# Kernel tuning notes

Hardware: AMD Instinct MI355X
Metric: run time of the kernel (lower is better)

## Reference

```python
import jax, jax.numpy as jnp
import numpy as np

NEG_SLOPE = 0.2
BN_EPS = 1e-5


def _gatv2(x, Wl, Wr, att, b, src, dst, N):
    # PyG GATv2Conv, concat=False: lin_l on source, lin_r on target,
    # e = a^T LeakyReLU(x_l[j] + x_r[i]); softmax over incoming edges of i;
    # out = mean_h( sum_j alpha_ij * x_l[j] ) + bias
    H, C = att.shape
    xl = (x @ Wl).reshape(N, H, C)
    xr = (x @ Wr).reshape(N, H, C)
    e = jax.nn.leaky_relu(xl[src] + xr[dst], NEG_SLOPE)          # [E,H,C]
    score = jnp.einsum('ehc,hc->eh', e, att)                     # [E,H]
    m = jax.ops.segment_max(score, dst, num_segments=N)          # [N,H]
    a = jnp.exp(score - m[dst])
    denom = jax.ops.segment_sum(a, dst, num_segments=N)
    alpha = a / denom[dst]                                       # [E,H]
    out = jax.ops.segment_sum(alpha[..., None] * xl[src], dst, num_segments=N)  # [N,H,C]
    return out.mean(axis=1) + b


def _bn(h, g, be):
    # BatchNorm1d, training-mode statistics (biased variance)
    mu = h.mean(axis=0)
    var = h.var(axis=0)
    return g * (h - mu) * jax.lax.rsqrt(var + BN_EPS) + be


def _gelu(x):
    return jax.nn.gelu(x, approximate=False)


def setup_inputs() -> dict:
    key = jax.random.key(0)
    N, F, HID, LAT, H, E, G = 50000, 64, 64, 64, 4, 800000, 256
    ks = jax.random.split(key, 32)
    d = {}
    d['x'] = jax.random.normal(ks[0], (N, F), dtype=jnp.float32)
    d['edge_src'] = jax.random.randint(ks[1], (E,), 0, N, dtype=jnp.int32)
    d['edge_dst'] = jax.random.randint(ks[2], (E,), 0, N, dtype=jnp.int32)
    d['batch'] = jnp.sort(jax.random.randint(ks[3], (N,), 0, G, dtype=jnp.int32))
    d['num_graphs'] = G
    def lin(k, fi, fo):
        return jax.random.normal(k, (fi, fo), dtype=jnp.float32) / np.sqrt(fi)
    i = 4
    for L, fin in zip((1, 2, 3), (F, HID, HID)):
        d[f'Wl{L}'] = lin(ks[i], fin, H * HID); i += 1
        d[f'Wr{L}'] = lin(ks[i], fin, H * HID); i += 1
        d[f'att{L}'] = jax.random.normal(ks[i], (H, HID), dtype=jnp.float32) / np.sqrt(HID); i += 1
        d[f'b{L}'] = jnp.zeros((HID,), dtype=jnp.float32)
        d[f'g{L}'] = jax.random.uniform(ks[i], (HID,), dtype=jnp.float32, minval=0.5, maxval=1.5); i += 1
        d[f'be{L}'] = 0.1 * jax.random.normal(ks[i], (HID,), dtype=jnp.float32); i += 1
    d['Wmu'] = lin(ks[i], HID, LAT); i += 1
    d['bmu'] = jnp.zeros((LAT,), dtype=jnp.float32)
    d['Wlv'] = lin(ks[i], HID, LAT); i += 1
    d['blv'] = jnp.zeros((LAT,), dtype=jnp.float32)
    return d


def reference(x, edge_src, edge_dst, batch, num_graphs,
              Wl1, Wr1, att1, b1, g1, be1,
              Wl2, Wr2, att2, b2, g2, be2,
              Wl3, Wr3, att3, b3, g3, be3,
              Wmu, bmu, Wlv, blv):
    N = x.shape[0]
    loops = jnp.arange(N, dtype=edge_src.dtype)
    src = jnp.concatenate([edge_src, loops])  # add_self_loops=True (PyG default)
    dst = jnp.concatenate([edge_dst, loops])

    h = _gelu(_bn(_gatv2(x, Wl1, Wr1, att1, b1, src, dst, N), g1, be1))
    h_in = h
    h = _gelu(_bn(_gatv2(h, Wl2, Wr2, att2, b2, src, dst, N), g2, be2)) + h_in
    h_in = h
    h = _gelu(_bn(_gatv2(h, Wl3, Wr3, att3, b3, src, dst, N), g3, be3)) + h_in

    h_pool = jax.ops.segment_sum(h, batch, num_segments=num_graphs)  # global_add_pool
    return (h_pool @ Wmu + bmu, h_pool @ Wlv + blv)
```

## Files before the change

### kernel.cpp

```cpp
#include <hip/hip_runtime.h>
#include <math.h>

typedef __attribute__((ext_vector_type(8))) short bf16x8;
typedef __attribute__((ext_vector_type(4))) float f32x4;
typedef __attribute__((ext_vector_type(2))) float f32x2;

static __device__ __forceinline__ unsigned short f2bf(float f) {
  unsigned u = __float_as_uint(f);
  unsigned r = (u + 0x7FFF + ((u >> 16) & 1)) >> 16;
  return (unsigned short)r;
}

#define DPP_ADD(x, ctrl) \
  ((x) + __int_as_float(__builtin_amdgcn_update_dpp(0, __float_as_int(x), (ctrl), 0xf, 0xf, true)))

#define NSHARD 64
#define NEB 256
#define ECAP 6144


__global__ __launch_bounds__(256) void k_prep(const float* __restrict__ W0, const float* __restrict__ W1,
                                              const float* __restrict__ W2, const float* __restrict__ W3,
                                              const float* __restrict__ W4, const float* __restrict__ W5,
                                              unsigned short* __restrict__ wt,
                                              const int* __restrict__ esrc,
                                              const int* __restrict__ edst,
                                              int* __restrict__ bktcnt,
                                              int2* __restrict__ ebuf, int E, int N) {
  if (blockIdx.x < 384) {
    int gid = blockIdx.x * 256 + threadIdx.x;
    int m = gid >> 14;
    int r = gid & 16383;
    int k = r >> 8;
    int n = r & 255;
    const float* W = (m == 0) ? W0 : (m == 1) ? W1 : (m == 2) ? W2
                   : (m == 3) ? W3 : (m == 4) ? W4 : W5;
    wt[(size_t)m * 16384 + n * 64 + k] = f2bf(W[k * 256 + n]);
    return;
  }
  const int b = blockIdx.x - 384;
  const int nbk = (N + 255) >> 8;
  __shared__ int cnt[256], base[256];
  cnt[threadIdx.x] = 0;
  __syncthreads();
  const int chunk = (E + NEB - 1) / NEB;
  const int e0 = b * chunk, e1 = min(e0 + chunk, E);
  for (int e = e0 + threadIdx.x; e < e1; e += 256) atomicAdd(&cnt[edst[e] >> 8], 1);
  __syncthreads();
  if (threadIdx.x < nbk && cnt[threadIdx.x])
    base[threadIdx.x] = atomicAdd(&bktcnt[threadIdx.x], cnt[threadIdx.x]);
  cnt[threadIdx.x] = 0;
  __syncthreads();
  for (int e = e0 + threadIdx.x; e < e1; e += 256) {
    int d = edst[e];
    int bk = d >> 8;
    int p = base[bk] + atomicAdd(&cnt[bk], 1);
    ebuf[(size_t)bk * ECAP + p] = make_int2(d, esrc[e]);
  }
}


static __device__ __forceinline__ void csr_pass2(const int2* __restrict__ ebuf,
                                                 const int* __restrict__ bktcnt,
                                                 int* __restrict__ rowptr,
                                                 int* __restrict__ colb,
                                                 int* __restrict__ ccur,
                                                 int N, char* smem) {
  const int b = blockIdx.x;
  const int nbk = (N + 255) >> 8;
  if (b >= nbk) return;
  int* hist = (int*)smem;
  int* s = (int*)smem + 256;
  int* sb = (int*)smem + 512;
  const int tid = threadIdx.x;
  const int lo = b * ECAP;
  const int hi = lo + bktcnt[b];
  hist[tid] = 0;
  __syncthreads();
  for (int i = lo + tid; i < hi; i += 256) atomicAdd(&hist[ebuf[i].x & 255], 1);
  __syncthreads();
  int deg = hist[tid];
  int pd = (deg + 3) & ~3;
  s[tid] = pd;
  __syncthreads();
  for (int off = 1; off < 256; off <<= 1) {
    int t = (tid >= off) ? s[tid - off] : 0;
    __syncthreads();
    s[tid] += t;
    __syncthreads();
  }
  if (tid == 255) sb[0] = atomicAdd(ccur, s[255]);
  __syncthreads();
  int pos = sb[0] + s[tid] - pd;
  int node = (b << 8) + tid;
  if (node < N) rowptr[node] = (int)((unsigned)pos | ((unsigned)deg << 22));
  hist[tid] = pos;
  __syncthreads();
  for (int i = lo + tid; i < hi; i += 256) {
    int2 e = ebuf[i];
    int p = atomicAdd(&hist[e.x & 255], 1);
    colb[p] = e.y << 8;
  }
}


static __device__ __forceinline__ void mm_gemm(const float* __restrict__ src,
                                               const float* __restrict__ bnsums,
                                               const float* __restrict__ g,
                                               const float* __restrict__ be,
                                               const float* __restrict__ resid,
                                               float* __restrict__ hout,
                                               const unsigned short* __restrict__ wt,
                                               unsigned char* __restrict__ xlb,
                                               unsigned char* __restrict__ xrb,
                                               int N, int ntiles, float inv_n,
                                               char* smem) {
  unsigned short* Bs = (unsigned short*)smem;
  unsigned short* Ah = (unsigned short*)(smem + 32768);
  const int t = threadIdx.x;
  const unsigned short* wb = wt + (blockIdx.y ? 16384 : 0);
  unsigned char* dst = blockIdx.y ? xrb : xlb;

  const int wave = t >> 6, lane = t & 63;
  const int rw = (wave & 1) * 16, cw = (wave >> 1) * 128;
  const int m15 = lane & 15, quad = lane >> 4;
  const int arow = t >> 3, ac0 = (t & 7) * 8;
  const int aoff = arow * 64 + (((t & 7) ^ (arow & 7)) << 3);

  float scale[8], shift[8];
  if (bnsums) {
    float* stat = (float*)smem;
    if (t < 128) {
      float a = 0.f;
#pragma unroll
      for (int sd = 0; sd < NSHARD; ++sd) a += bnsums[sd * 128 + t];
      stat[t] = a;
    }
    __syncthreads();
#pragma unroll
    for (int i = 0; i < 8; ++i) {
      int c = ac0 + i;
      float mu = stat[c] * inv_n;
      float var = stat[64 + c] * inv_n - mu * mu;
      float rs = rsqrtf(var + 1e-5f) * g[c];
      scale[i] = rs;
      shift[i] = be[c] - mu * rs;
    }
    __syncthreads();
  }

#pragma unroll
  for (int j = 0; j < 8; ++j) {
    int cidx = t + 256 * j;
    int n = cidx >> 3, gg = cidx & 7;
    *(bf16x8*)&Bs[n * 64 + (((gg ^ ((n >> 3) & 7))) << 3)] =
        *(const bf16x8*)(wb + (size_t)n * 64 + gg * 8);
  }

  const bool wr_h = (hout != nullptr) && (blockIdx.y == 0);
  const int gstride = gridDim.x;

  float4 a0, a1, rv0, rv1;
  auto loadA = [&](int tl, float4& x0, float4& x1, float4& r0v, float4& r1v) {
    x0 = make_float4(0.f, 0.f, 0.f, 0.f);
    x1 = make_float4(0.f, 0.f, 0.f, 0.f);
    r0v = make_float4(0.f, 0.f, 0.f, 0.f);
    r1v = make_float4(0.f, 0.f, 0.f, 0.f);
    int gr = tl * 32 + arow;
    if (tl < ntiles && gr < N) {
      x0 = *(const float4*)(src + (size_t)gr * 64 + ac0);
      x1 = *(const float4*)(src + (size_t)gr * 64 + ac0 + 4);
      if (resid) {
        r0v = *(const float4*)(resid + (size_t)gr * 64 + ac0);
        r1v = *(const float4*)(resid + (size_t)gr * 64 + ac0 + 4);
      }
    }
  };
  loadA(blockIdx.x, a0, a1, rv0, rv1);

  for (int tile = blockIdx.x; tile < ntiles; tile += gstride) {
    int r0 = tile * 32;
    int gr = r0 + arow;
    {
      float vs[8] = {a0.x, a0.y, a0.z, a0.w, a1.x, a1.y, a1.z, a1.w};
      if (bnsums) {
        float rv[8] = {rv0.x, rv0.y, rv0.z, rv0.w, rv1.x, rv1.y, rv1.z, rv1.w};
#pragma unroll
        for (int i = 0; i < 8; ++i) {
          float v = fmaf(vs[i], scale[i], shift[i]);
          float ge = 0.5f * v * (1.f + erff(v * 0.70710678118654752f));
          vs[i] = ge + rv[i];
        }
        if (wr_h && gr < N) {
          float4 o0 = {vs[0], vs[1], vs[2], vs[3]};
          float4 o1 = {vs[4], vs[5], vs[6], vs[7]};
          *(float4*)(hout + (size_t)gr * 64 + ac0) = o0;
          *(float4*)(hout + (size_t)gr * 64 + ac0 + 4) = o1;
        }
      }
      bf16x8 hi8;
#pragma unroll
      for (int i = 0; i < 8; ++i) hi8[i] = (short)f2bf(vs[i]);
      *(bf16x8*)&Ah[aoff] = hi8;
    }
    __syncthreads();

    loadA(tile + gstride, a0, a1, rv0, rv1);

    f32x4 acc[8];
#pragma unroll
    for (int s = 0; s < 8; ++s) acc[s] = (f32x4){0.f, 0.f, 0.f, 0.f};
    const int xq = m15 & 7;
#pragma unroll
    for (int kk = 0; kk < 64; kk += 32) {
      const int ga = (((kk >> 3) + quad) ^ xq) << 3;
      bf16x8 ah = *(const bf16x8*)&Ah[(rw + m15) * 64 + ga];
#pragma unroll
      for (int s = 0; s < 8; ++s) {
        bf16x8 b = *(const bf16x8*)&Bs[(cw + m15 * 8 + s) * 64 + ga];
        acc[s] = __builtin_amdgcn_mfma_f32_16x16x32_bf16(ah, b, acc[s], 0, 0, 0);
      }
    }
#pragma unroll
    for (int r = 0; r < 4; ++r) {
      int row_g = r0 + rw + quad * 4 + r;
      if (row_g < N) {
        int w0 = __builtin_amdgcn_cvt_pk_fp8_f32(acc[0][r], acc[1][r], 0, false);
        w0 = __builtin_amdgcn_cvt_pk_fp8_f32(acc[2][r], acc[3][r], w0, true);
        int w1 = __builtin_amdgcn_cvt_pk_fp8_f32(acc[4][r], acc[5][r], 0, false);
        w1 = __builtin_amdgcn_cvt_pk_fp8_f32(acc[6][r], acc[7][r], w1, true);
        uint2 o = {(unsigned)w0, (unsigned)w1};
        *(uint2*)(dst + (size_t)row_g * 256 + cw + m15 * 8) = o;
      }
    }
    __syncthreads();
  }
}

__global__ __launch_bounds__(256, 4) void k_mm0(const float* __restrict__ src,
                                                const unsigned short* __restrict__ wt,
                                                unsigned char* __restrict__ xlb,
                                                unsigned char* __restrict__ xrb,
                                                const int2* __restrict__ ebuf,
                                                const int* __restrict__ bktcnt,
                                                int* __restrict__ rowptr,
                                                int* __restrict__ colb,
                                                int* __restrict__ ccur,
                                                int N, int ntiles) {
  __shared__ __align__(16) char smem[36864];
  if (blockIdx.y == 2) {
    csr_pass2(ebuf, bktcnt, rowptr, colb, ccur, N, smem);
    return;
  }
  mm_gemm(src, nullptr, nullptr, nullptr, nullptr, nullptr, wt, xlb, xrb, N, ntiles, 0.f, smem);
}

__global__ __launch_bounds__(256, 4) void k_mm1(const float* __restrict__ src,
                                                const float* __restrict__ bnsums,
                                                const float* __restrict__ g,
                                                const float* __restrict__ be,
                                                float* __restrict__ hout,
                                                const unsigned short* __restrict__ wt,
                                                unsigned char* __restrict__ xlb,
                                                unsigned char* __restrict__ xrb,
                                                int N, int ntiles, float inv_n) {
  __shared__ __align__(16) char smem[36864];
  mm_gemm(src, bnsums, g, be, nullptr, hout, wt, xlb, xrb, N, ntiles, inv_n, smem);
}

__global__ __launch_bounds__(256, 4) void k_mm2(const float* __restrict__ src,
                                                const float* __restrict__ bnsums,
                                                const float* __restrict__ g,
                                                const float* __restrict__ be,
                                                const float* __restrict__ resid,
                                                float* __restrict__ hout,
                                                const unsigned short* __restrict__ wt,
                                                unsigned char* __restrict__ xlb,
                                                unsigned char* __restrict__ xrb,
                                                int N, int ntiles, float inv_n) {
  __shared__ __align__(16) char smem[36864];
  mm_gemm(src, bnsums, g, be, resid, hout, wt, xlb, xrb, N, ntiles, inv_n, smem);
}


static __device__ __forceinline__ void gat_body(const unsigned char* __restrict__ xlb,
                                                const unsigned char* __restrict__ xrb,
                                                const float* __restrict__ att,
                                                const float* __restrict__ bias,
                                                const int* __restrict__ rowptr,
                                                const int* __restrict__ colb,
                                                float* __restrict__ out,
                                                float* __restrict__ bnsums, int N) {
  __shared__ float sres[4][64];
  const int lane = threadIdx.x & 63;
  const int wv = threadIdx.x >> 6;
  const int half = lane >> 5;
  const int l5 = lane & 31;
  const int node0 = blockIdx.x * 4 + wv;
  const bool valid = node0 < N;
  const int node = __builtin_amdgcn_readfirstlane(valid ? node0 : 0);
  const int rp = rowptr[node];
  const int beg = rp & 0x3FFFFF;
  const int deg = (int)(((unsigned)rp) >> 22);
  const int end = valid ? beg + deg : beg;

  const unsigned char* xl = xlb;
  const unsigned lb = (unsigned)l5 * 8u;

  auto sel = [&](int a, int b) { return (unsigned)(half ? b : a); };

  int4 c0 = *(const int4*)(colb + beg);
  int4 c1 = *(const int4*)(colb + beg + 4);
  const unsigned self_off = (unsigned)(node << 8);
  uint2 vbs = *(const uint2*)(xl + self_off + lb);
  uint2 pd0 = *(const uint2*)(xl + (sel(c0.x, c0.y) + lb));
  uint2 pd1 = *(const uint2*)(xl + (sel(c0.z, c0.w) + lb));
  uint2 pt0 = *(const uint2*)(xl + (sel(c1.x, c1.y) + lb));
  uint2 pt1 = *(const uint2*)(xl + (sel(c1.z, c1.w) + lb));
  int4 cn = *(const int4*)(colb + beg + 8);

  float4 aa = *(const float4*)(att + l5 * 8);
  float4 ab = *(const float4*)(att + l5 * 8 + 4);
  const float LOG2E = 1.4426950408889634f;
  const f32x2 a01 = {aa.x * LOG2E, aa.y * LOG2E};
  const f32x2 a23 = {aa.z * LOG2E, aa.w * LOG2E};
  const f32x2 a45 = {ab.x * LOG2E, ab.y * LOG2E};
  const f32x2 a67 = {ab.z * LOG2E, ab.w * LOG2E};
  const f32x2 c02 = {0.2f, 0.2f};
  uint2 xru = *(const uint2*)(xrb + self_off + lb);
  const f32x2 xr01 = __builtin_amdgcn_cvt_pk_f32_fp8((int)xru.x, false);
  const f32x2 xr23 = __builtin_amdgcn_cvt_pk_f32_fp8((int)xru.x, true);
  const f32x2 xr45 = __builtin_amdgcn_cvt_pk_f32_fp8((int)xru.y, false);
  const f32x2 xr67 = __builtin_amdgcn_cvt_pk_f32_fp8((int)xru.y, true);

  auto score = [&](uint2 vb, f32x2& v01, f32x2& v23, f32x2& v45, f32x2& v67) -> float {
    v01 = __builtin_amdgcn_cvt_pk_f32_fp8((int)vb.x, false);
    v23 = __builtin_amdgcn_cvt_pk_f32_fp8((int)vb.x, true);
    v45 = __builtin_amdgcn_cvt_pk_f32_fp8((int)vb.y, false);
    v67 = __builtin_amdgcn_cvt_pk_f32_fp8((int)vb.y, true);
    f32x2 s01 = v01 + xr01;
    f32x2 s23 = v23 + xr23;
    f32x2 s45 = v45 + xr45;
    f32x2 s67 = v67 + xr67;
    s01 = __builtin_elementwise_max(s01, s01 * c02);
    s23 = __builtin_elementwise_max(s23, s23 * c02);
    s45 = __builtin_elementwise_max(s45, s45 * c02);
    s67 = __builtin_elementwise_max(s67, s67 * c02);
    f32x2 q = s01 * a01;
    q = __builtin_elementwise_fma(s23, a23, q);
    q = __builtin_elementwise_fma(s45, a45, q);
    q = __builtin_elementwise_fma(s67, a67, q);
    float p = q.x + q.y;
    p = DPP_ADD(p, 0xB1);
    p = DPP_ADD(p, 0x4E);
    p = DPP_ADD(p, 0x141);
    return p;
  };

  f32x2 sv01, sv23, sv45, sv67;
  const float m = score(vbs, sv01, sv23, sv45, sv67);

  const float hsel = half ? 0.f : 1.f;
  float lsum = hsel;
  const f32x2 hs2 = {hsel, hsel};
  f32x2 o01 = sv01 * hs2, o23 = sv23 * hs2, o45 = sv45 * hs2, o67 = sv67 * hs2;

  auto proc = [&](uint2 vb, int ebase) {
    f32x2 v01, v23, v45, v67;
    float p = score(vb, v01, v23, v45, v67);
    float w = __builtin_amdgcn_exp2f(fminf(p - m, 126.f));
    w = (ebase + half < end) ? w : 0.f;
    lsum += w;
    f32x2 w2 = {w, w};
    o01 = __builtin_elementwise_fma(w2, v01, o01);
    o23 = __builtin_elementwise_fma(w2, v23, o23);
    o45 = __builtin_elementwise_fma(w2, v45, o45);
    o67 = __builtin_elementwise_fma(w2, v67, o67);
  };

  for (int e = beg; e < end; e += 4) {
    uint2 pu0 = *(const uint2*)(xl + (sel(cn.x, cn.y) + lb));
    uint2 pu1 = *(const uint2*)(xl + (sel(cn.z, cn.w) + lb));
    cn = *(const int4*)(colb + e + 12);
    proc(pd0, e);
    proc(pd1, e + 2);
    pd0 = pt0; pd1 = pt1;
    pt0 = pu0; pt1 = pu1;
  }

  lsum += __shfl_xor(lsum, 32, 64);
  float inv = __builtin_amdgcn_rcpf(lsum);
  float r[8] = {o01.x * inv, o01.y * inv, o23.x * inv, o23.y * inv,
                o45.x * inv, o45.y * inv, o67.x * inv, o67.y * inv};
#pragma unroll
  for (int j = 0; j < 8; ++j) {
    r[j] += __shfl_xor(r[j], 8, 64);
    r[j] += __shfl_xor(r[j], 16, 64);
    r[j] += __shfl_xor(r[j], 32, 64);
  }
  if (lane < 8) {
    float4 res0 = {0.f, 0.f, 0.f, 0.f}, res1 = {0.f, 0.f, 0.f, 0.f};
    if (valid) {
      float4 b0 = *(const float4*)(bias + lane * 8);
      float4 b1 = *(const float4*)(bias + lane * 8 + 4);
      res0.x = 0.25f * r[0] + b0.x;
      res0.y = 0.25f * r[1] + b0.y;
      res0.z = 0.25f * r[2] + b0.z;
      res0.w = 0.25f * r[3] + b0.w;
      res1.x = 0.25f * r[4] + b1.x;
      res1.y = 0.25f * r[5] + b1.y;
      res1.z = 0.25f * r[6] + b1.z;
      res1.w = 0.25f * r[7] + b1.w;
      *(float4*)(out + (size_t)node * 64 + lane * 8) = res0;
      *(float4*)(out + (size_t)node * 64 + lane * 8 + 4) = res1;
    }
    *(float4*)&sres[wv][lane * 8] = res0;
    *(float4*)&sres[wv][lane * 8 + 4] = res1;
  }
  __syncthreads();
  if (threadIdx.x < 64) {
    int c = threadIdx.x;
    float s0 = sres[0][c], s1 = sres[1][c], s2 = sres[2][c], s3 = sres[3][c];
    float* bs = bnsums + (size_t)(blockIdx.x & (NSHARD - 1)) * 128;
    atomicAdd(&bs[c], s0 + s1 + s2 + s3);
    atomicAdd(&bs[64 + c], s0 * s0 + s1 * s1 + s2 * s2 + s3 * s3);
  }
}

__global__ __launch_bounds__(256) void k_gat0(const unsigned char* __restrict__ xlb,
                                              const unsigned char* __restrict__ xrb,
                                              const float* __restrict__ att,
                                              const float* __restrict__ bias,
                                              const int* __restrict__ rowptr,
                                              const int* __restrict__ colb,
                                              float* __restrict__ out,
                                              float* __restrict__ bnsums, int N) {
  gat_body(xlb, xrb, att, bias, rowptr, colb, out, bnsums, N);
}
__global__ __launch_bounds__(256) void k_gat1(const unsigned char* __restrict__ xlb,
                                              const unsigned char* __restrict__ xrb,
                                              const float* __restrict__ att,
                                              const float* __restrict__ bias,
                                              const int* __restrict__ rowptr,
                                              const int* __restrict__ colb,
                                              float* __restrict__ out,
                                              float* __restrict__ bnsums, int N) {
  gat_body(xlb, xrb, att, bias, rowptr, colb, out, bnsums, N);
}
__global__ __launch_bounds__(256) void k_gat2(const unsigned char* __restrict__ xlb,
                                              const unsigned char* __restrict__ xrb,
                                              const float* __restrict__ att,
                                              const float* __restrict__ bias,
                                              const int* __restrict__ rowptr,
                                              const int* __restrict__ colb,
                                              float* __restrict__ out,
                                              float* __restrict__ bnsums, int N) {
  gat_body(xlb, xrb, att, bias, rowptr, colb, out, bnsums, N);
}


__global__ __launch_bounds__(256) void k_bn_pool(const float* __restrict__ gat,
                                                 const float* __restrict__ bnsums,
                                                 const float* __restrict__ g,
                                                 const float* __restrict__ be,
                                                 const float* __restrict__ resid,
                                                 const int* __restrict__ batch,
                                                 float* __restrict__ pool,
                                                 int N, float inv_n) {
  __shared__ float sc[64], sh[64];
  if (threadIdx.x < 64) {
    int c = threadIdx.x;
    float s = 0.f, q = 0.f;
    for (int sd = 0; sd < NSHARD; ++sd) {
      s += bnsums[sd * 128 + c];
      q += bnsums[sd * 128 + 64 + c];
    }
    float mu = s * inv_n;
    float var = q * inv_n - mu * mu;
    float rs = rsqrtf(var + 1e-5f) * g[c];
    sc[c] = rs;
    sh[c] = be[c] - mu * rs;
  }
  __syncthreads();
  const int c = threadIdx.x & 63;
  const int wv = threadIdx.x >> 6;
  int n0 = (blockIdx.x * 4 + wv) * 32;
  if (n0 >= N) return;
  int n1 = min(n0 + 32, N);
  int curg = batch[n0];
  float acc = 0.f;
  for (int n = n0; n < n1; ++n) {
    int b = batch[n];
    if (b != curg) {
      atomicAdd(&pool[(size_t)curg * 64 + c], acc);
      acc = 0.f;
      curg = b;
    }
    float v = fmaf(gat[(size_t)n * 64 + c], sc[c], sh[c]);
    float ge = 0.5f * v * (1.f + erff(v * 0.70710678118654752f));
    acc += ge + resid[(size_t)n * 64 + c];
  }
  atomicAdd(&pool[(size_t)curg * 64 + c], acc);
}


__global__ void k_head(const float* __restrict__ pool, const float* __restrict__ Wmu,
                       const float* __restrict__ bmu, const float* __restrict__ Wlv,
                       const float* __restrict__ blv, float* __restrict__ out, int G) {
  int g = blockIdx.x;
  int c = threadIdx.x;
  __shared__ float row[64];
  row[c] = pool[(size_t)g * 64 + c];
  __syncthreads();
  float am = 0.f, al = 0.f;
  for (int k = 0; k < 64; ++k) {
    float r = row[k];
    am = fmaf(r, Wmu[k * 64 + c], am);
    al = fmaf(r, Wlv[k * 64 + c], al);
  }
  out[(size_t)g * 64 + c] = am + bmu[c];
  out[(size_t)G * 64 + (size_t)g * 64 + c] = al + blv[c];
}


extern "C" void kernel_launch(void* const* d_in, const int* in_sizes, int n_in,
                              void* d_out, int out_size, void* d_ws, size_t ws_size,
                              hipStream_t stream) {
  const float* x    = (const float*)d_in[0];
  const int* esrc   = (const int*)d_in[1];
  const int* edst   = (const int*)d_in[2];
  const int* batch  = (const int*)d_in[3];
  const float* Wl[3]  = {(const float*)d_in[5],  (const float*)d_in[11], (const float*)d_in[17]};
  const float* Wr[3]  = {(const float*)d_in[6],  (const float*)d_in[12], (const float*)d_in[18]};
  const float* att[3] = {(const float*)d_in[7],  (const float*)d_in[13], (const float*)d_in[19]};
  const float* bia[3] = {(const float*)d_in[8],  (const float*)d_in[14], (const float*)d_in[20]};
  const float* gam[3] = {(const float*)d_in[9],  (const float*)d_in[15], (const float*)d_in[21]};
  const float* bet[3] = {(const float*)d_in[10], (const float*)d_in[16], (const float*)d_in[22]};
  const float* Wmu = (const float*)d_in[23];
  const float* bmu = (const float*)d_in[24];
  const float* Wlv = (const float*)d_in[25];
  const float* blv = (const float*)d_in[26];
  float* out = (float*)d_out;

  const int N = in_sizes[0] / 64;
  const int E = in_sizes[1];
  const int G = out_size / 128;
  const int nbk = (N + 255) / 256;

  char* p = (char*)d_ws;
  auto alloc = [&](size_t bytes) -> void* {
    void* r = (void*)p;
    p += (bytes + 255) & ~(size_t)255;
    return r;
  };
  int*   bktcnt  = (int*)alloc(256 * 4);
  float* bnsums  = (float*)alloc(3 * NSHARD * 128 * 4);
  float* pool    = (float*)alloc((size_t)G * 64 * 4);
  int*   ccur    = (int*)alloc(256);
  int*   colb    = (int*)alloc(((size_t)E + 3 * (size_t)N + 64) * 4);
  char*  zend    = p;
  unsigned char* xlb = (unsigned char*)alloc((size_t)N * 256);
  unsigned char* xrb = (unsigned char*)alloc((size_t)N * 256);
  float* hA     = (float*)alloc((size_t)N * 64 * 4);
  float* hB     = (float*)alloc((size_t)N * 64 * 4);
  float* gat    = (float*)alloc((size_t)N * 64 * 4);
  int*   rowptr = (int*)alloc((size_t)(N + 1) * 4);
  int2*  ebuf   = (int2*)alloc((size_t)nbk * ECAP * 8);
  unsigned short* wt = (unsigned short*)alloc(6 * 16384 * 2);

  const int nbGat = (N + 3) / 4;
  const int ntiles = (N + 31) / 32;
  const float inv_n = 1.f / (float)N;

  hipMemsetAsync(bktcnt, 0, (size_t)(zend - (char*)bktcnt), stream);

  k_prep<<<384 + NEB, 256, 0, stream>>>(Wl[0], Wr[0], Wl[1], Wr[1], Wl[2], Wr[2], wt,
                                        esrc, edst, bktcnt, ebuf, E, N);

  float* bns0 = bnsums;
  float* bns1 = bnsums + NSHARD * 128;
  float* bns2 = bnsums + 2 * NSHARD * 128;

  k_mm0<<<dim3(512, 3), 256, 0, stream>>>(x, wt, xlb, xrb, ebuf, bktcnt, rowptr, colb,
                                          ccur, N, ntiles);
  k_gat0<<<nbGat, 256, 0, stream>>>(xlb, xrb, att[0], bia[0], rowptr, colb, gat, bns0, N);
  k_mm1<<<dim3(512, 2), 256, 0, stream>>>(gat, bns0, gam[0], bet[0], hA,
                                          wt + 2 * 16384, xlb, xrb, N, ntiles, inv_n);
  k_gat1<<<nbGat, 256, 0, stream>>>(xlb, xrb, att[1], bia[1], rowptr, colb, gat, bns1, N);
  k_mm2<<<dim3(512, 2), 256, 0, stream>>>(gat, bns1, gam[1], bet[1], hA, hB,
                                          wt + 4 * 16384, xlb, xrb, N, ntiles, inv_n);
  k_gat2<<<nbGat, 256, 0, stream>>>(xlb, xrb, att[2], bia[2], rowptr, colb, gat, bns2, N);
  k_bn_pool<<<(N + 127) / 128, 256, 0, stream>>>(gat, bns2, gam[2], bet[2], hB, batch, pool,
                                                 N, inv_n);
  k_head<<<G, 64, 0, stream>>>(pool, Wmu, bmu, Wlv, blv, out, G);
}
```

Before: 358.1 us.

## Fuse left and right projection GEMMs into one block pass

Each GEMM block now loads both the Wl and Wr weight tiles into shared memory and computes xl and xr together from a single staged A tile. Previously the two projections ran as separate grid-y slices, and each slice re-read the input and redid the BN/GELU/residual preprocessing. This halves the A-side loads and the normalization work. In exchange, shared memory per block doubles to about 68KB, launch bounds drop to 2 blocks per CU, and the accumulator register count doubles.

```diff
diff --git a/kernel.cpp b/kernel.cpp
--- a/kernel.cpp
+++ b/kernel.cpp
@@ -116,10 +116,8 @@
                                                int N, int ntiles, float inv_n,
                                                char* smem) {
   unsigned short* Bs = (unsigned short*)smem;
-  unsigned short* Ah = (unsigned short*)(smem + 32768);
+  unsigned short* Ah = (unsigned short*)(smem + 65536);
   const int t = threadIdx.x;
-  const unsigned short* wb = wt + (blockIdx.y ? 16384 : 0);
-  unsigned char* dst = blockIdx.y ? xrb : xlb;
 
   const int wave = t >> 6, lane = t & 63;
   const int rw = (wave & 1) * 16, cw = (wave >> 1) * 128;
@@ -150,14 +148,14 @@
   }
 
 #pragma unroll
-  for (int j = 0; j < 8; ++j) {
+  for (int j = 0; j < 16; ++j) {
     int cidx = t + 256 * j;
     int n = cidx >> 3, gg = cidx & 7;
     *(bf16x8*)&Bs[n * 64 + (((gg ^ ((n >> 3) & 7))) << 3)] =
-        *(const bf16x8*)(wb + (size_t)n * 64 + gg * 8);
-  }
-
-  const bool wr_h = (hout != nullptr) && (blockIdx.y == 0);
+        *(const bf16x8*)(wt + (size_t)n * 64 + gg * 8);
+  }
+
+  const bool wr_h = (hout != nullptr);
   const int gstride = gridDim.x;
 
   float4 a0, a1, rv0, rv1;
@@ -207,9 +205,12 @@
 
     loadA(tile + gstride, a0, a1, rv0, rv1);
 
-    f32x4 acc[8];
-#pragma unroll
-    for (int s = 0; s < 8; ++s) acc[s] = (f32x4){0.f, 0.f, 0.f, 0.f};
+    f32x4 accL[8], accR[8];
+#pragma unroll
+    for (int s = 0; s < 8; ++s) {
+      accL[s] = (f32x4){0.f, 0.f, 0.f, 0.f};
+      accR[s] = (f32x4){0.f, 0.f, 0.f, 0.f};
+    }
     const int xq = m15 & 7;
 #pragma unroll
     for (int kk = 0; kk < 64; kk += 32) {
@@ -217,27 +218,35 @@
       bf16x8 ah = *(const bf16x8*)&Ah[(rw + m15) * 64 + ga];
 #pragma unroll
       for (int s = 0; s < 8; ++s) {
-        bf16x8 b = *(const bf16x8*)&Bs[(cw + m15 * 8 + s) * 64 + ga];
-        acc[s] = __builtin_amdgcn_mfma_f32_16x16x32_bf16(ah, b, acc[s], 0, 0, 0);
+        bf16x8 bl = *(const bf16x8*)&Bs[(cw + m15 * 8 + s) * 64 + ga];
+        accL[s] = __builtin_amdgcn_mfma_f32_16x16x32_bf16(ah, bl, accL[s], 0, 0, 0);
+        bf16x8 br = *(const bf16x8*)&Bs[(256 + cw + m15 * 8 + s) * 64 + ga];
+        accR[s] = __builtin_amdgcn_mfma_f32_16x16x32_bf16(ah, br, accR[s], 0, 0, 0);
       }
     }
 #pragma unroll
     for (int r = 0; r < 4; ++r) {
       int row_g = r0 + rw + quad * 4 + r;
       if (row_g < N) {
-        int w0 = __builtin_amdgcn_cvt_pk_fp8_f32(acc[0][r], acc[1][r], 0, false);
-        w0 = __builtin_amdgcn_cvt_pk_fp8_f32(acc[2][r], acc[3][r], w0, true);
-        int w1 = __builtin_amdgcn_cvt_pk_fp8_f32(acc[4][r], acc[5][r], 0, false);
-        w1 = __builtin_amdgcn_cvt_pk_fp8_f32(acc[6][r], acc[7][r], w1, true);
-        uint2 o = {(unsigned)w0, (unsigned)w1};
-        *(uint2*)(dst + (size_t)row_g * 256 + cw + m15 * 8) = o;
+        int w0 = __builtin_amdgcn_cvt_pk_fp8_f32(accL[0][r], accL[1][r], 0, false);
+        w0 = __builtin_amdgcn_cvt_pk_fp8_f32(accL[2][r], accL[3][r], w0, true);
+        int w1 = __builtin_amdgcn_cvt_pk_fp8_f32(accL[4][r], accL[5][r], 0, false);
+        w1 = __builtin_amdgcn_cvt_pk_fp8_f32(accL[6][r], accL[7][r], w1, true);
+        uint2 oL = {(unsigned)w0, (unsigned)w1};
+        *(uint2*)(xlb + (size_t)row_g * 256 + cw + m15 * 8) = oL;
+        int w2 = __builtin_amdgcn_cvt_pk_fp8_f32(accR[0][r], accR[1][r], 0, false);
+        w2 = __builtin_amdgcn_cvt_pk_fp8_f32(accR[2][r], accR[3][r], w2, true);
+        int w3 = __builtin_amdgcn_cvt_pk_fp8_f32(accR[4][r], accR[5][r], 0, false);
+        w3 = __builtin_amdgcn_cvt_pk_fp8_f32(accR[6][r], accR[7][r], w3, true);
+        uint2 oR = {(unsigned)w2, (unsigned)w3};
+        *(uint2*)(xrb + (size_t)row_g * 256 + cw + m15 * 8) = oR;
       }
     }
     __syncthreads();
   }
 }
 
-__global__ __launch_bounds__(256, 4) void k_mm0(const float* __restrict__ src,
+__global__ __launch_bounds__(256, 2) void k_mm0(const float* __restrict__ src,
                                                 const unsigned short* __restrict__ wt,
                                                 unsigned char* __restrict__ xlb,
                                                 unsigned char* __restrict__ xrb,
@@ -247,15 +256,15 @@
                                                 int* __restrict__ colb,
                                                 int* __restrict__ ccur,
                                                 int N, int ntiles) {
-  __shared__ __align__(16) char smem[36864];
-  if (blockIdx.y == 2) {
+  __shared__ __align__(16) char smem[69632];
+  if (blockIdx.y == 1) {
     csr_pass2(ebuf, bktcnt, rowptr, colb, ccur, N, smem);
     return;
   }
   mm_gemm(src, nullptr, nullptr, nullptr, nullptr, nullptr, wt, xlb, xrb, N, ntiles, 0.f, smem);
 }
 
-__global__ __launch_bounds__(256, 4) void k_mm1(const float* __restrict__ src,
+__global__ __launch_bounds__(256, 2) void k_mm1(const float* __restrict__ src,
                                                 const float* __restrict__ bnsums,
                                                 const float* __restrict__ g,
                                                 const float* __restrict__ be,
@@ -264,11 +273,11 @@
                                                 unsigned char* __restrict__ xlb,
                                                 unsigned char* __restrict__ xrb,
                                                 int N, int ntiles, float inv_n) {
-  __shared__ __align__(16) char smem[36864];
+  __shared__ __align__(16) char smem[69632];
   mm_gemm(src, bnsums, g, be, nullptr, hout, wt, xlb, xrb, N, ntiles, inv_n, smem);
 }
 
-__global__ __launch_bounds__(256, 4) void k_mm2(const float* __restrict__ src,
+__global__ __launch_bounds__(256, 2) void k_mm2(const float* __restrict__ src,
                                                 const float* __restrict__ bnsums,
                                                 const float* __restrict__ g,
                                                 const float* __restrict__ be,
@@ -278,7 +287,7 @@
                                                 unsigned char* __restrict__ xlb,
                                                 unsigned char* __restrict__ xrb,
                                                 int N, int ntiles, float inv_n) {
-  __shared__ __align__(16) char smem[36864];
+  __shared__ __align__(16) char smem[69632];
   mm_gemm(src, bnsums, g, be, resid, hout, wt, xlb, xrb, N, ntiles, inv_n, smem);
 }
 
@@ -581,13 +590,13 @@
   float* bns1 = bnsums + NSHARD * 128;
   float* bns2 = bnsums + 2 * NSHARD * 128;
 
-  k_mm0<<<dim3(512, 3), 256, 0, stream>>>(x, wt, xlb, xrb, ebuf, bktcnt, rowptr, colb,
+  k_mm0<<<dim3(512, 2), 256, 0, stream>>>(x, wt, xlb, xrb, ebuf, bktcnt, rowptr, colb,
                                           ccur, N, ntiles);
   k_gat0<<<nbGat, 256, 0, stream>>>(xlb, xrb, att[0], bia[0], rowptr, colb, gat, bns0, N);
-  k_mm1<<<dim3(512, 2), 256, 0, stream>>>(gat, bns0, gam[0], bet[0], hA,
+  k_mm1<<<dim3(512, 1), 256, 0, stream>>>(gat, bns0, gam[0], bet[0], hA,
                                           wt + 2 * 16384, xlb, xrb, N, ntiles, inv_n);
   k_gat1<<<nbGat, 256, 0, stream>>>(xlb, xrb, att[1], bia[1], rowptr, colb, gat, bns1, N);
-  k_mm2<<<dim3(512, 2), 256, 0, stream>>>(gat, bns1, gam[1], bet[1], hA, hB,
+  k_mm2<<<dim3(512, 1), 256, 0, stream>>>(gat, bns1, gam[1], bet[1], hA, hB,
                                           wt + 4 * 16384, xlb, xrb, N, ntiles, inv_n);
   k_gat2<<<nbGat, 256, 0, stream>>>(xlb, xrb, att[2], bia[2], rowptr, colb, gat, bns2, N);
   k_bn_pool<<<(N + 127) / 128, 256, 0, stream>>>(gat, bns2, gam[2], bet[2], hB, batch, pool,
```

After: 365.2 us. No clear change (+2.0%).
